# Performance work log

Measured on AMD Instinct MI355X. Metric: run time of the kernel, lower is better.

## Reference

```python
import jax, jax.numpy as jnp
import numpy as np
import math

CHANNELS = 512
OUT_CHANNELS = 512
N_HEADS = 8
WINDOW = 4
K_CH = CHANNELS // N_HEADS


def _conv1x1(x, W, b):
    # x: (B, C_in, T), W: (C_out, C_in), b: (C_out,)
    return jnp.einsum('oc,bct->bot', W, x) + b[None, :, None]


def _get_relative_embeddings(emb, length, window=WINDOW):
    # emb: (H, 2*window+1, k_ch) -> (H, 2*length-1, k_ch)
    pad_length = max(length - (window + 1), 0)
    start = max(window + 1 - length, 0)
    e = jnp.pad(emb, ((0, 0), (pad_length, pad_length), (0, 0))) if pad_length > 0 else emb
    return e[:, start:start + 2 * length - 1]


def _relative_to_absolute(x):
    # x: (B, H, L, 2L-1) -> (B, H, L, L)
    b, h, L, _ = x.shape
    x = jnp.pad(x, ((0, 0), (0, 0), (0, 0), (0, 1)))          # (B,H,L,2L)
    xf = x.reshape(b, h, L * 2 * L)
    xf = jnp.pad(xf, ((0, 0), (0, 0), (L - 1, 0)))
    return xf.reshape(b, h, L + 1, 2 * L - 1)[:, :, :L, L - 1:]


def _absolute_to_relative(x):
    # x: (B, H, L, L) -> (B, H, L, 2L-1)
    b, h, L, _ = x.shape
    x = jnp.pad(x, ((0, 0), (0, 0), (0, 0), (0, L - 1)))       # (B,H,L,2L-1)
    xf = x.reshape(b, h, L * (2 * L - 1))
    xf = jnp.pad(xf, ((0, 0), (0, 0), (L, 0)))
    return xf.reshape(b, h, L, 2 * L)[:, :, :, 1:]


def setup_inputs() -> dict:
    key = jax.random.key(0)
    ks = jax.random.split(key, 16)
    B, C, T = 4, CHANNELS, 1024
    xavier = math.sqrt(2.0 / (C + C))
    rel_std = K_CH ** -0.5
    return {
        'x_q': jax.random.normal(ks[0], (B, C, T), jnp.float32),
        'x_k': jax.random.normal(ks[1], (B, C, T), jnp.float32),
        'x_v': jax.random.normal(ks[2], (B, C, T), jnp.float32),
        'Wq': jax.random.normal(ks[3], (C, C), jnp.float32) * xavier,
        'bq': jnp.zeros((C,), jnp.float32),
        'Wk': jax.random.normal(ks[4], (C, C), jnp.float32) * xavier,
        'bk': jnp.zeros((C,), jnp.float32),
        'Wv': jax.random.normal(ks[5], (C, C), jnp.float32) * xavier,
        'bv': jnp.zeros((C,), jnp.float32),
        'Wo': jax.random.normal(ks[6], (OUT_CHANNELS, C), jnp.float32) * xavier,
        'bo': jnp.zeros((OUT_CHANNELS,), jnp.float32),
        'emb_rel_k': jax.random.normal(ks[7], (N_HEADS, 2 * WINDOW + 1, K_CH), jnp.float32) * rel_std,
        'emb_rel_v': jax.random.normal(ks[8], (N_HEADS, 2 * WINDOW + 1, K_CH), jnp.float32) * rel_std,
    }


def reference(x_q, x_k, x_v, Wq, bq, Wk, bk, Wv, bv, Wo, bo, emb_rel_k, emb_rel_v):
    q = _conv1x1(x_q, Wq, bq)
    k = _conv1x1(x_k, Wk, bk)
    v = _conv1x1(x_v, Wv, bv)
    B, C, T = q.shape
    # (B, C, T) -> (B, H, T, k_ch); head h owns contiguous k_ch channel chunk
    qh = q.reshape(B, N_HEADS, K_CH, T).transpose(0, 1, 3, 2) / math.sqrt(K_CH)
    kh = k.reshape(B, N_HEADS, K_CH, T).transpose(0, 1, 3, 2)
    vh = v.reshape(B, N_HEADS, K_CH, T).transpose(0, 1, 3, 2)
    scores = jnp.einsum('bhtd,bhsd->bhts', qh, kh)              # (B,H,T,T)
    rel_k = _get_relative_embeddings(emb_rel_k, T)              # (H,2T-1,d)
    rel_logits = jnp.einsum('bhtd,hmd->bhtm', qh, rel_k)        # (B,H,T,2T-1)
    scores = scores + _relative_to_absolute(rel_logits)
    attn = jax.nn.softmax(scores, axis=-1)
    ctx = jnp.einsum('bhts,bhsd->bhtd', attn, vh)
    rel_w = _absolute_to_relative(attn)                         # (B,H,T,2T-1)
    rel_v = _get_relative_embeddings(emb_rel_v, T)
    ctx = ctx + jnp.einsum('bhtm,hmd->bhtd', rel_w, rel_v)
    out = ctx.transpose(0, 1, 3, 2).reshape(B, C, T)
    return _conv1x1(out, Wo, bo)
```

## Files before the change

kernel.cpp:

```cpp
#include <hip/hip_runtime.h>

#define T_LEN 1024
#define NH 8
#define DH 64
#define CCH 512
#define LOG2E 1.44269504088896340736f

typedef _Float16 f16;
typedef _Float16 f16x8 __attribute__((ext_vector_type(8)));
typedef _Float16 f16x4 __attribute__((ext_vector_type(4)));
typedef float f32x4 __attribute__((ext_vector_type(4)));

__device__ __forceinline__ void dma16(const void* g, void* l)
{
    __builtin_amdgcn_global_load_lds((const __attribute__((address_space(1))) void*)g,
                                     (__attribute__((address_space(3))) void*)l, 16, 0, 0);
}

__global__ __launch_bounds__(256)
void prep_kernel(const float* __restrict__ x0, const float* __restrict__ x1,
                 const float* __restrict__ x2, const float* __restrict__ W0,
                 const float* __restrict__ W1, const float* __restrict__ W2,
                 const float* __restrict__ W3, f16* __restrict__ o0,
                 f16* __restrict__ o1, f16* __restrict__ o2, f16* __restrict__ w0,
                 f16* __restrict__ w1, f16* __restrict__ w2, f16* __restrict__ w3,
                 int B)
{
    const int z = blockIdx.z;
    if (z < 3 * B) {
        const int t0 = blockIdx.x * 64, c0 = blockIdx.y * 64;
        const int which = z / B, b = z % B;
        const float* x = (which == 0) ? x0 : (which == 1) ? x1 : x2;
        f16* o = (which == 0) ? o0 : (which == 1) ? o1 : o2;

        __shared__ float L[64 * 68];
        const int cl = threadIdx.x & 63, g = threadIdx.x >> 6;
        const float* src = x + ((size_t)(b * CCH + c0 + cl)) * T_LEN + t0 + g * 16;
        #pragma unroll
        for (int j = 0; j < 4; ++j)
            *(float4*)&L[cl * 68 + g * 16 + 4 * j] = *(const float4*)&src[4 * j];
        __syncthreads();
        const int tl = threadIdx.x & 63, cg = (threadIdx.x >> 6) * 16;
        f16 h[16];
        #pragma unroll
        for (int j = 0; j < 16; ++j) h[j] = (f16)L[(cg + j) * 68 + tl];
        f16* dst = o + ((size_t)(b * T_LEN + t0 + tl)) * CCH + c0 + cg;
        *(f16x8*)&dst[0] = *(f16x8*)&h[0];
        *(f16x8*)&dst[8] = *(f16x8*)&h[8];
    } else {
        const int slice = z - 3 * B;
        size_t i = ((size_t)(slice * 128 + blockIdx.y * 16 + blockIdx.x) * 256 + threadIdx.x) * 4;
        const int wi = (int)(i >> 18);
        const size_t off = i & 262143;
        const float* src = (wi == 0) ? W0 : (wi == 1) ? W1 : (wi == 2) ? W2 : W3;
        f16* dst = (wi == 0) ? w0 : (wi == 1) ? w1 : (wi == 2) ? w2 : w3;
        float4 v4 = *(const float4*)&src[off];
        f16x4 h = {(f16)v4.x, (f16)v4.y, (f16)v4.z, (f16)v4.w};
        *(f16x4*)&dst[off] = h;
    }
}

__global__ __launch_bounds__(256)
void proj_qkv(const f16* __restrict__ xq, const f16* __restrict__ xk,
              const f16* __restrict__ xv, const f16* __restrict__ wq,
              const f16* __restrict__ wk, const f16* __restrict__ wv,
              const float* __restrict__ bq, const float* __restrict__ bk,
              const float* __restrict__ bv, f16* __restrict__ qo,
              f16* __restrict__ ko, f16* __restrict__ vo)
{
    const int which = blockIdx.z;
    const f16* X = (which == 0) ? xq : (which == 1) ? xk : xv;
    const f16* W = (which == 0) ? wq : (which == 1) ? wk : wv;
    const float* bias = (which == 0) ? bq : (which == 1) ? bk : bv;
    const float scale = (which == 0) ? 0.125f * LOG2E : 1.0f;

    const int r0 = blockIdx.x * 128;
    const int o0 = blockIdx.y * 64;
    const int tid = threadIdx.x;
    const int w = tid >> 6, lane = tid & 63;
    const int quad = lane >> 4, l15 = lane & 15;

    __shared__ __align__(16) f16 Xs[2][128 * 64];
    __shared__ __align__(16) f16 Ws[2][64 * 64];

    const int srow = tid >> 3;
    const int scol = ((tid & 7) ^ (srow & 7)) << 3;

    const f16* Xg = X + (size_t)(r0 + srow) * CCH + scol;
    const f16* Wg = W + (size_t)(o0 + srow) * CCH + scol;

    #pragma unroll
    for (int j = 0; j < 4; ++j)
        dma16(Xg + (size_t)(32 * j) * CCH, &Xs[0][(size_t)tid * 8 + j * 2048]);
    #pragma unroll
    for (int j = 0; j < 2; ++j)
        dma16(Wg + (size_t)(32 * j) * CCH, &Ws[0][(size_t)tid * 8 + j * 2048]);

    f32x4 acc[8] = {};

    for (int kc = 0; kc < 8; ++kc) {
        __syncthreads();
        if (kc < 7) {
            const int bf = (kc + 1) & 1, c1 = (kc + 1) * 64;
            #pragma unroll
            for (int j = 0; j < 4; ++j)
                dma16(Xg + c1 + (size_t)(32 * j) * CCH, &Xs[bf][(size_t)tid * 8 + j * 2048]);
            #pragma unroll
            for (int j = 0; j < 2; ++j)
                dma16(Wg + c1 + (size_t)(32 * j) * CCH, &Ws[bf][(size_t)tid * 8 + j * 2048]);
        }
        const int cb = kc & 1;
        #pragma unroll
        for (int ks = 0; ks < 2; ++ks) {
            const int sl = ((ks * 4 + quad) ^ (l15 & 7)) << 3;
            f16x8 xf[2], wf[4];
            #pragma unroll
            for (int im = 0; im < 2; ++im)
                xf[im] = *(const f16x8*)&Xs[cb][(32 * w + 16 * im + l15) * 64 + sl];
            #pragma unroll
            for (int cm = 0; cm < 4; ++cm)
                wf[cm] = *(const f16x8*)&Ws[cb][(16 * cm + l15) * 64 + sl];
            if (which < 2) {
                #pragma unroll
                for (int im = 0; im < 2; ++im)
                    #pragma unroll
                    for (int cm = 0; cm < 4; ++cm)
                        acc[im * 4 + cm] = __builtin_amdgcn_mfma_f32_16x16x32_f16(
                            xf[im], wf[cm], acc[im * 4 + cm], 0, 0, 0);
            } else {
                #pragma unroll
                for (int cm = 0; cm < 4; ++cm)
                    #pragma unroll
                    for (int in = 0; in < 2; ++in)
                        acc[cm * 2 + in] = __builtin_amdgcn_mfma_f32_16x16x32_f16(
                            wf[cm], xf[in], acc[cm * 2 + in], 0, 0, 0);
            }
        }
    }

    if (which < 2) {
        f16* out = (which == 0) ? qo : ko;
        float bl[4];
        #pragma unroll
        for (int cm = 0; cm < 4; ++cm) bl[cm] = bias[o0 + 16 * cm + l15];
        #pragma unroll
        for (int im = 0; im < 2; ++im)
            #pragma unroll
            for (int r = 0; r < 4; ++r) {
                size_t row = (size_t)(r0 + 32 * w + 16 * im + 4 * quad + r) * CCH;
                #pragma unroll
                for (int cm = 0; cm < 4; ++cm)
                    out[row + o0 + 16 * cm + l15] =
                        (f16)((acc[im * 4 + cm][r] + bl[cm]) * scale);
            }
    } else {
        const int bb = r0 >> 10, tb = r0 & 1023;
        #pragma unroll
        for (int cm = 0; cm < 4; ++cm) {
            float4 bv4 = *(const float4*)&bias[o0 + 16 * cm + 4 * quad];
            float bl[4] = {bv4.x, bv4.y, bv4.z, bv4.w};
            #pragma unroll
            for (int r = 0; r < 4; ++r) {
                size_t row = ((size_t)(bb * CCH + o0 + 16 * cm + 4 * quad + r)) * T_LEN;
                #pragma unroll
                for (int in = 0; in < 2; ++in)
                    vo[row + tb + 32 * w + 16 * in + l15] =
                        (f16)(acc[cm * 2 + in][r] + bl[r]);
            }
        }
    }
}

__global__ __launch_bounds__(256)
void attn_mfma(const f16* __restrict__ q, const f16* __restrict__ kk,
               const f16* __restrict__ v, const float* __restrict__ ekg,
               const float* __restrict__ evg, f16* __restrict__ ctx)
{
    const int t0 = blockIdx.x * 64, h = blockIdx.y, b = blockIdx.z;
    const int tid = threadIdx.x;
    const int w = tid >> 6, lane = tid & 63;
    const int quad = lane >> 4, l15 = lane & 15;

    __shared__ __align__(16) f16 Qs[4096], Ps[4096];
    __shared__ __align__(16) f16 Ks[2][4096], Vs[2][4096];
    __shared__ float eks[576], evs[576];
    __shared__ float ls[64];

    const int srow = tid >> 3;
    const int scol = ((tid & 7) ^ (srow & 7)) << 3;

    for (int i = tid; i < 576; i += 256) {
        eks[i] = ekg[h * 576 + i];
        evs[i] = evg[h * 576 + i];
    }

    const f16* gk = kk + ((size_t)(b * T_LEN + srow)) * CCH + h * DH + scol;
    const f16* gv = v + ((size_t)(b * CCH + h * DH + srow)) * T_LEN + scol;

    dma16(q + ((size_t)(b * T_LEN + t0 + srow)) * CCH + h * DH + scol, &Qs[(size_t)tid * 8]);
    dma16(q + ((size_t)(b * T_LEN + t0 + srow + 32)) * CCH + h * DH + scol, &Qs[((size_t)tid + 256) * 8]);
    dma16(gk, &Ks[0][(size_t)tid * 8]);
    dma16(gk + (size_t)32 * CCH, &Ks[0][((size_t)tid + 256) * 8]);
    dma16(gv, &Vs[0][(size_t)tid * 8]);
    dma16(gv + (size_t)32 * T_LEN, &Vs[0][((size_t)tid + 256) * 8]);
    __syncthreads();

    f16x8 qf[2];
    #pragma unroll
    for (int ks = 0; ks < 2; ++ks)
        qf[ks] = *(const f16x8*)&Qs[(16 * w + l15) * 64 + (((ks * 4 + quad) ^ (l15 & 7)) << 3)];

    const int myt = 16 * w + l15;
    float Ssum = 0.f;
    f32x4 O[4] = {};

    const bool corner_hi = (blockIdx.x == 0);
    const bool corner_lo = (blockIdx.x == 15);

    for (int it = 0; it < 16; ++it) {
        const int kb = it, cb = it & 1;
        if (it) __syncthreads();

        f32x4 S[4] = {};
        #pragma unroll
        for (int ks = 0; ks < 2; ++ks) {
            #pragma unroll
            for (int ct = 0; ct < 4; ++ct) {
                f16x8 a = *(const f16x8*)&Ks[cb][(16 * ct + l15) * 64 + (((ks * 4 + quad) ^ (l15 & 7)) << 3)];
                S[ct] = __builtin_amdgcn_mfma_f32_16x16x32_f16(a, qf[ks], S[ct], 0, 0, 0);
            }
        }

        if ((corner_hi && kb == 15) || (corner_lo && kb == 0)) {
            const int s0g = kb * 64;
            #pragma unroll
            for (int ct = 0; ct < 4; ++ct)
                #pragma unroll
                for (int r = 0; r < 4; ++r) {
                    int t_g = t0 + myt;
                    int s_g = s0g + 16 * ct + 4 * quad + r;
                    int df = s_g - t_g;
                    if (df >= 1019 && df <= 1023) {
                        const float* ekp = &eks[(df - 1019) * 64];
                        float sacc = 0.f;
                        for (int d = 0; d < 64; ++d)
                            sacc += (float)Qs[myt * 64 + (((d >> 3) ^ (myt & 7)) << 3) + (d & 7)] * ekp[d];
                        S[ct][r] += sacc;
                    } else if (df >= -1023 && df <= -1021) {
                        const float* ekp = &eks[(1029 + df) * 64];
                        const int t2 = myt - 1;
                        float sacc = 0.f;
                        for (int d = 0; d < 64; ++d)
                            sacc += (float)Qs[t2 * 64 + (((d >> 3) ^ (t2 & 7)) << 3) + (d & 7)] * ekp[d];
                        S[ct][r] += sacc;
                    }
                }
        }

        #pragma unroll
        for (int ct = 0; ct < 4; ++ct) {
            f16x4 pk_;
            #pragma unroll
            for (int r = 0; r < 4; ++r) {
                float p = exp2f(S[ct][r]);
                Ssum += p;
                pk_[r] = (f16)p;
            }
            int colh = (((2 * ct + (quad >> 1)) ^ (myt & 7)) << 3) + (quad & 1) * 4;
            *(f16x4*)&Ps[myt * 64 + colh] = pk_;
        }
        __syncthreads();

        if (it < 15) {
            const int nb = cb ^ 1;
            dma16(gk + (size_t)((it + 1) * 64) * CCH, &Ks[nb][(size_t)tid * 8]);
            dma16(gk + (size_t)((it + 1) * 64 + 32) * CCH, &Ks[nb][((size_t)tid + 256) * 8]);
            dma16(gv + (it + 1) * 64, &Vs[nb][(size_t)tid * 8]);
            dma16(gv + (size_t)32 * T_LEN + (it + 1) * 64, &Vs[nb][((size_t)tid + 256) * 8]);
        }

        #pragma unroll
        for (int ks = 0; ks < 2; ++ks) {
            f16x8 a = *(const f16x8*)&Ps[(16 * w + l15) * 64 + (((ks * 4 + quad) ^ (l15 & 7)) << 3)];
            #pragma unroll
            for (int ct = 0; ct < 4; ++ct) {
                f16x8 bf = *(const f16x8*)&Vs[cb][(16 * ct + l15) * 64 + (((ks * 4 + quad) ^ (l15 & 7)) << 3)];
                O[ct] = __builtin_amdgcn_mfma_f32_16x16x32_f16(a, bf, O[ct], 0, 0, 0);
            }
        }

        const int s0g = kb * 64;
        if (s0g <= t0 + 67 && s0g + 63 >= t0 - 4) {
            #pragma unroll
            for (int r = 0; r < 4; ++r) {
                int t_loc = 16 * w + 4 * quad + r;
                int t_g = t0 + t_loc;
                int slo = max(s0g, t_g - 4), shi = min(s0g + 63, t_g + 4);
                for (int s = slo; s <= shi; ++s) {
                    int sl = s - s0g;
                    float p = (float)Ps[t_loc * 64 + (((sl >> 3) ^ (t_loc & 7)) << 3) + (sl & 7)];
                    const float* evp = &evs[(s - t_g + 4) * 64];
                    #pragma unroll
                    for (int ct = 0; ct < 4; ++ct)
                        O[ct][r] += p * evp[16 * ct + l15];
                }
            }
        }
    }

    Ssum += __shfl_xor(Ssum, 16);
    Ssum += __shfl_xor(Ssum, 32);
    if (quad == 0) ls[myt] = 1.0f / Ssum;
    __syncthreads();

    #pragma unroll
    for (int r = 0; r < 4; ++r) {
        const int t_loc = 16 * w + 4 * quad + r;
        const float rl = ls[t_loc];
        size_t rowo = ((size_t)(b * T_LEN + t0 + t_loc)) * CCH + h * DH;
        #pragma unroll
        for (int ct = 0; ct < 4; ++ct)
            ctx[rowo + 16 * ct + l15] = (f16)(O[ct][r] * rl);
    }
}

__global__ __launch_bounds__(256)
void proj_out(const f16* __restrict__ ctx, const f16* __restrict__ Wo,
              const float* __restrict__ bo, float* __restrict__ out)
{
    const int r0 = blockIdx.x * 64;
    const int o0 = blockIdx.y * 64;
    const int tid = threadIdx.x;
    const int w = tid >> 6, lane = tid & 63;
    const int quad = lane >> 4, l15 = lane & 15;

    __shared__ __align__(16) f16 Cs[2][4096];
    __shared__ __align__(16) f16 Ws[2][4096];

    const int srow = tid >> 3;
    const int scol = ((tid & 7) ^ (srow & 7)) << 3;

    const f16* Cg = ctx + (size_t)(r0 + srow) * CCH + scol;
    const f16* Wg = Wo + (size_t)(o0 + srow) * CCH + scol;

    dma16(Cg, &Cs[0][(size_t)tid * 8]);
    dma16(Cg + (size_t)32 * CCH, &Cs[0][((size_t)tid + 256) * 8]);
    dma16(Wg, &Ws[0][(size_t)tid * 8]);
    dma16(Wg + (size_t)32 * CCH, &Ws[0][((size_t)tid + 256) * 8]);

    f32x4 acc[4] = {};

    for (int kc = 0; kc < 8; ++kc) {
        __syncthreads();
        if (kc < 7) {
            const int bf = (kc + 1) & 1, c1 = (kc + 1) * 64;
            dma16(Cg + c1, &Cs[bf][(size_t)tid * 8]);
            dma16(Cg + c1 + (size_t)32 * CCH, &Cs[bf][((size_t)tid + 256) * 8]);
            dma16(Wg + c1, &Ws[bf][(size_t)tid * 8]);
            dma16(Wg + c1 + (size_t)32 * CCH, &Ws[bf][((size_t)tid + 256) * 8]);
        }
        const int cb = kc & 1;
        #pragma unroll
        for (int ks = 0; ks < 2; ++ks) {
            const int sl = ((ks * 4 + quad) ^ (l15 & 7)) << 3;
            f16x8 cf = *(const f16x8*)&Cs[cb][(16 * w + l15) * 64 + sl];
            #pragma unroll
            for (int cm = 0; cm < 4; ++cm) {
                f16x8 wf = *(const f16x8*)&Ws[cb][(16 * cm + l15) * 64 + sl];
                acc[cm] = __builtin_amdgcn_mfma_f32_16x16x32_f16(wf, cf, acc[cm], 0, 0, 0);
            }
        }
    }

    const int bb = r0 >> 10, tb = r0 & 1023;
    #pragma unroll
    for (int cm = 0; cm < 4; ++cm) {
        float4 bv4 = *(const float4*)&bo[o0 + 16 * cm + 4 * quad];
        float bl[4] = {bv4.x, bv4.y, bv4.z, bv4.w};
        #pragma unroll
        for (int r = 0; r < 4; ++r) {
            size_t row = ((size_t)(bb * CCH + o0 + 16 * cm + 4 * quad + r)) * T_LEN;
            out[row + tb + 16 * w + l15] = acc[cm][r] + bl[r];
        }
    }
}

extern "C" void kernel_launch(void* const* d_in, const int* in_sizes, int n_in,
                              void* d_out, int out_size, void* d_ws, size_t ws_size,
                              hipStream_t stream)
{
    const float* x_q = (const float*)d_in[0];
    const float* x_k = (const float*)d_in[1];
    const float* x_v = (const float*)d_in[2];
    const float* Wq  = (const float*)d_in[3];
    const float* bq  = (const float*)d_in[4];
    const float* Wk  = (const float*)d_in[5];
    const float* bk  = (const float*)d_in[6];
    const float* Wv  = (const float*)d_in[7];
    const float* bv  = (const float*)d_in[8];
    const float* Wo  = (const float*)d_in[9];
    const float* bo  = (const float*)d_in[10];
    const float* erk = (const float*)d_in[11];
    const float* erv = (const float*)d_in[12];

    const int B = in_sizes[0] / (CCH * T_LEN);
    const size_t te = (size_t)B * CCH * T_LEN;
    const size_t we = (size_t)CCH * CCH;

    f16* p = (f16*)d_ws;
    f16* xTq = p; p += te;
    f16* xTk = p; p += te;
    f16* xTv = p; p += te;
    f16* wqh = p; p += we;
    f16* wkh = p; p += we;
    f16* wvh = p; p += we;
    f16* woh = p; p += we;
    f16* qh  = p; p += te;
    f16* kh  = p; p += te;
    f16* vh  = p; p += te;
    f16* ch  = p; p += te;

    dim3 blk(256);
    prep_kernel<<<dim3(16, 8, 3 * B + 8), blk, 0, stream>>>(
        x_q, x_k, x_v, Wq, Wk, Wv, Wo, xTq, xTk, xTv, wqh, wkh, wvh, woh, B);
    proj_qkv<<<dim3(B * 8, 8, 3), blk, 0, stream>>>(
        xTq, xTk, xTv, wqh, wkh, wvh, bq, bk, bv, qh, kh, vh);
    attn_mfma<<<dim3(T_LEN / 64, NH, B), blk, 0, stream>>>(
        qh, kh, vh, erk, erv, ch);
    proj_out<<<dim3(B * 16, 8), blk, 0, stream>>>(
        ch, woh, bo, (float*)d_out);
}
```

Baseline: 152.7 us.

## Load activation fragments directly into registers and hoist K/V prefetch in attention

In the QKV and output projection kernels, the activation operand is no longer staged through LDS. Each wave loads its own MFMA fragments straight from global memory into registers, prefetching the next k-chunk one iteration ahead, while weights stay double-buffered in LDS. This cuts LDS footprint and traffic, at the cost of more register pressure and uncoalesced-ish 16-byte global loads. In attention, the next K/V tile DMA is issued at the top of the iteration and one barrier between the P write and the PV product is removed. Dropping that barrier risks reading Ps rows before they are written, though each wave appears to read only its own rows.

```diff
diff --git a/kernel.cpp b/kernel.cpp
--- a/kernel.cpp
+++ b/kernel.cpp
@@ -80,21 +80,22 @@
     const int w = tid >> 6, lane = tid & 63;
     const int quad = lane >> 4, l15 = lane & 15;
 
-    __shared__ __align__(16) f16 Xs[2][128 * 64];
-    __shared__ __align__(16) f16 Ws[2][64 * 64];
+    __shared__ __align__(16) f16 Ws[2][4096];
 
     const int srow = tid >> 3;
     const int scol = ((tid & 7) ^ (srow & 7)) << 3;
-
-    const f16* Xg = X + (size_t)(r0 + srow) * CCH + scol;
     const f16* Wg = W + (size_t)(o0 + srow) * CCH + scol;
 
+    dma16(Wg, &Ws[0][(size_t)tid * 8]);
+    dma16(Wg + (size_t)32 * CCH, &Ws[0][((size_t)tid + 256) * 8]);
+
+    const f16* xp = X + (size_t)(r0 + 32 * w + l15) * CCH + quad * 8;
+    f16x8 xf[2][2];
     #pragma unroll
-    for (int j = 0; j < 4; ++j)
-        dma16(Xg + (size_t)(32 * j) * CCH, &Xs[0][(size_t)tid * 8 + j * 2048]);
-    #pragma unroll
-    for (int j = 0; j < 2; ++j)
-        dma16(Wg + (size_t)(32 * j) * CCH, &Ws[0][(size_t)tid * 8 + j * 2048]);
+    for (int ks = 0; ks < 2; ++ks)
+        #pragma unroll
+        for (int im = 0; im < 2; ++im)
+            xf[ks][im] = *(const f16x8*)&xp[(size_t)(16 * im) * CCH + ks * 32];
 
     f32x4 acc[8] = {};
 
@@ -102,21 +103,22 @@
         __syncthreads();
         if (kc < 7) {
             const int bf = (kc + 1) & 1, c1 = (kc + 1) * 64;
-            #pragma unroll
-            for (int j = 0; j < 4; ++j)
-                dma16(Xg + c1 + (size_t)(32 * j) * CCH, &Xs[bf][(size_t)tid * 8 + j * 2048]);
-            #pragma unroll
-            for (int j = 0; j < 2; ++j)
-                dma16(Wg + c1 + (size_t)(32 * j) * CCH, &Ws[bf][(size_t)tid * 8 + j * 2048]);
-        }
+            dma16(Wg + c1, &Ws[bf][(size_t)tid * 8]);
+            dma16(Wg + c1 + (size_t)32 * CCH, &Ws[bf][((size_t)tid + 256) * 8]);
+        }
+        const int nk = ((kc + 1) & 7) * 64;
+        f16x8 xn[2][2];
+        #pragma unroll
+        for (int ks = 0; ks < 2; ++ks)
+            #pragma unroll
+            for (int im = 0; im < 2; ++im)
+                xn[ks][im] = *(const f16x8*)&xp[(size_t)(16 * im) * CCH + nk + ks * 32];
+
         const int cb = kc & 1;
         #pragma unroll
         for (int ks = 0; ks < 2; ++ks) {
             const int sl = ((ks * 4 + quad) ^ (l15 & 7)) << 3;
-            f16x8 xf[2], wf[4];
-            #pragma unroll
-            for (int im = 0; im < 2; ++im)
-                xf[im] = *(const f16x8*)&Xs[cb][(32 * w + 16 * im + l15) * 64 + sl];
+            f16x8 wf[4];
             #pragma unroll
             for (int cm = 0; cm < 4; ++cm)
                 wf[cm] = *(const f16x8*)&Ws[cb][(16 * cm + l15) * 64 + sl];
@@ -126,16 +128,21 @@
                     #pragma unroll
                     for (int cm = 0; cm < 4; ++cm)
                         acc[im * 4 + cm] = __builtin_amdgcn_mfma_f32_16x16x32_f16(
-                            xf[im], wf[cm], acc[im * 4 + cm], 0, 0, 0);
+                            xf[ks][im], wf[cm], acc[im * 4 + cm], 0, 0, 0);
             } else {
                 #pragma unroll
                 for (int cm = 0; cm < 4; ++cm)
                     #pragma unroll
                     for (int in = 0; in < 2; ++in)
                         acc[cm * 2 + in] = __builtin_amdgcn_mfma_f32_16x16x32_f16(
-                            wf[cm], xf[in], acc[cm * 2 + in], 0, 0, 0);
-            }
-        }
+                            wf[cm], xf[ks][in], acc[cm * 2 + in], 0, 0, 0);
+            }
+        }
+        #pragma unroll
+        for (int ks = 0; ks < 2; ++ks)
+            #pragma unroll
+            for (int im = 0; im < 2; ++im)
+                xf[ks][im] = xn[ks][im];
     }
 
     if (which < 2) {
@@ -220,6 +227,14 @@
     for (int it = 0; it < 16; ++it) {
         const int kb = it, cb = it & 1;
         if (it) __syncthreads();
+
+        if (it < 15) {
+            const int nb = cb ^ 1;
+            dma16(gk + (size_t)((it + 1) * 64) * CCH, &Ks[nb][(size_t)tid * 8]);
+            dma16(gk + (size_t)((it + 1) * 64 + 32) * CCH, &Ks[nb][((size_t)tid + 256) * 8]);
+            dma16(gv + (it + 1) * 64, &Vs[nb][(size_t)tid * 8]);
+            dma16(gv + (size_t)32 * T_LEN + (it + 1) * 64, &Vs[nb][((size_t)tid + 256) * 8]);
+        }
 
         f32x4 S[4] = {};
         #pragma unroll
@@ -269,15 +284,6 @@
             int colh = (((2 * ct + (quad >> 1)) ^ (myt & 7)) << 3) + (quad & 1) * 4;
             *(f16x4*)&Ps[myt * 64 + colh] = pk_;
         }
-        __syncthreads();
-
-        if (it < 15) {
-            const int nb = cb ^ 1;
-            dma16(gk + (size_t)((it + 1) * 64) * CCH, &Ks[nb][(size_t)tid * 8]);
-            dma16(gk + (size_t)((it + 1) * 64 + 32) * CCH, &Ks[nb][((size_t)tid + 256) * 8]);
-            dma16(gv + (it + 1) * 64, &Vs[nb][(size_t)tid * 8]);
-            dma16(gv + (size_t)32 * T_LEN + (it + 1) * 64, &Vs[nb][((size_t)tid + 256) * 8]);
-        }
 
         #pragma unroll
         for (int ks = 0; ks < 2; ++ks) {
@@ -334,19 +340,20 @@
     const int w = tid >> 6, lane = tid & 63;
     const int quad = lane >> 4, l15 = lane & 15;
 
-    __shared__ __align__(16) f16 Cs[2][4096];
     __shared__ __align__(16) f16 Ws[2][4096];
 
     const int srow = tid >> 3;
     const int scol = ((tid & 7) ^ (srow & 7)) << 3;
-
-    const f16* Cg = ctx + (size_t)(r0 + srow) * CCH + scol;
     const f16* Wg = Wo + (size_t)(o0 + srow) * CCH + scol;
 
-    dma16(Cg, &Cs[0][(size_t)tid * 8]);
-    dma16(Cg + (size_t)32 * CCH, &Cs[0][((size_t)tid + 256) * 8]);
     dma16(Wg, &Ws[0][(size_t)tid * 8]);
     dma16(Wg + (size_t)32 * CCH, &Ws[0][((size_t)tid + 256) * 8]);
+
+    const f16* cp = ctx + (size_t)(r0 + 16 * w + l15) * CCH + quad * 8;
+    f16x8 cf[2];
+    #pragma unroll
+    for (int ks = 0; ks < 2; ++ks)
+        cf[ks] = *(const f16x8*)&cp[ks * 32];
 
     f32x4 acc[4] = {};
 
@@ -354,22 +361,27 @@
         __syncthreads();
         if (kc < 7) {
             const int bf = (kc + 1) & 1, c1 = (kc + 1) * 64;
-            dma16(Cg + c1, &Cs[bf][(size_t)tid * 8]);
-            dma16(Cg + c1 + (size_t)32 * CCH, &Cs[bf][((size_t)tid + 256) * 8]);
             dma16(Wg + c1, &Ws[bf][(size_t)tid * 8]);
             dma16(Wg + c1 + (size_t)32 * CCH, &Ws[bf][((size_t)tid + 256) * 8]);
         }
+        const int nk = ((kc + 1) & 7) * 64;
+        f16x8 cn[2];
+        #pragma unroll
+        for (int ks = 0; ks < 2; ++ks)
+            cn[ks] = *(const f16x8*)&cp[nk + ks * 32];
+
         const int cb = kc & 1;
         #pragma unroll
         for (int ks = 0; ks < 2; ++ks) {
             const int sl = ((ks * 4 + quad) ^ (l15 & 7)) << 3;
-            f16x8 cf = *(const f16x8*)&Cs[cb][(16 * w + l15) * 64 + sl];
             #pragma unroll
             for (int cm = 0; cm < 4; ++cm) {
                 f16x8 wf = *(const f16x8*)&Ws[cb][(16 * cm + l15) * 64 + sl];
-                acc[cm] = __builtin_amdgcn_mfma_f32_16x16x32_f16(wf, cf, acc[cm], 0, 0, 0);
-            }
-        }
+                acc[cm] = __builtin_amdgcn_mfma_f32_16x16x32_f16(wf, cf[ks], acc[cm], 0, 0, 0);
+            }
+        }
+        cf[0] = cn[0];
+        cf[1] = cn[1];
     }
 
     const int bb = r0 >> 10, tb = r0 & 1023;
```

New measurement: 152.7 us. About the same (-0.0%).

## Enlarge projection GEMM tiles to 128x128 and prefetch K/V earlier in attention

Applied to the files above, without the earlier changes.

The QKV and output projection kernels now use 128x128 output tiles, with each wave computing a 64x64 sub-tile (4x4 MFMAs). This raises operand reuse per LDS load but drops LDS double buffering in favour of load-then-sync per K chunk. The grids shrink accordingly, to 384 blocks for QKV and 128 for the output projection. In attention, the next K/V tile DMA is issued at the start of each iteration and the intermediate barrier before the PV product is removed, giving more overlap but risking a race on the Ps buffer writes versus reads.

```diff
diff --git a/kernel.cpp b/kernel.cpp
--- a/kernel.cpp
+++ b/kernel.cpp
@@ -75,13 +75,15 @@
     const float scale = (which == 0) ? 0.125f * LOG2E : 1.0f;
 
     const int r0 = blockIdx.x * 128;
-    const int o0 = blockIdx.y * 64;
+    const int o0 = blockIdx.y * 128;
     const int tid = threadIdx.x;
     const int w = tid >> 6, lane = tid & 63;
     const int quad = lane >> 4, l15 = lane & 15;
-
-    __shared__ __align__(16) f16 Xs[2][128 * 64];
-    __shared__ __align__(16) f16 Ws[2][64 * 64];
+    const int a  = w >> 1;
+    const int b2 = w & 1;
+
+    __shared__ __align__(16) f16 Xs[128 * 64];
+    __shared__ __align__(16) f16 Wsh[128 * 64];
 
     const int srow = tid >> 3;
     const int scol = ((tid & 7) ^ (srow & 7)) << 3;
@@ -89,51 +91,45 @@
     const f16* Xg = X + (size_t)(r0 + srow) * CCH + scol;
     const f16* Wg = W + (size_t)(o0 + srow) * CCH + scol;
 
-    #pragma unroll
-    for (int j = 0; j < 4; ++j)
-        dma16(Xg + (size_t)(32 * j) * CCH, &Xs[0][(size_t)tid * 8 + j * 2048]);
-    #pragma unroll
-    for (int j = 0; j < 2; ++j)
-        dma16(Wg + (size_t)(32 * j) * CCH, &Ws[0][(size_t)tid * 8 + j * 2048]);
-
-    f32x4 acc[8] = {};
+    const int ax = (which < 2) ? a : b2;
+    const int aw = (which < 2) ? b2 : a;
+
+    f32x4 acc[4][4] = {};
 
     for (int kc = 0; kc < 8; ++kc) {
+        if (kc) __syncthreads();
+        const int c1 = kc * 64;
+        #pragma unroll
+        for (int jj = 0; jj < 4; ++jj) {
+            dma16(Xg + c1 + (size_t)(32 * jj) * CCH, &Xs[((size_t)tid + 256 * jj) * 8]);
+            dma16(Wg + c1 + (size_t)(32 * jj) * CCH, &Wsh[((size_t)tid + 256 * jj) * 8]);
+        }
         __syncthreads();
-        if (kc < 7) {
-            const int bf = (kc + 1) & 1, c1 = (kc + 1) * 64;
-            #pragma unroll
-            for (int j = 0; j < 4; ++j)
-                dma16(Xg + c1 + (size_t)(32 * j) * CCH, &Xs[bf][(size_t)tid * 8 + j * 2048]);
-            #pragma unroll
-            for (int j = 0; j < 2; ++j)
-                dma16(Wg + c1 + (size_t)(32 * j) * CCH, &Ws[bf][(size_t)tid * 8 + j * 2048]);
-        }
-        const int cb = kc & 1;
+
         #pragma unroll
         for (int ks = 0; ks < 2; ++ks) {
             const int sl = ((ks * 4 + quad) ^ (l15 & 7)) << 3;
-            f16x8 xf[2], wf[4];
-            #pragma unroll
-            for (int im = 0; im < 2; ++im)
-                xf[im] = *(const f16x8*)&Xs[cb][(32 * w + 16 * im + l15) * 64 + sl];
-            #pragma unroll
-            for (int cm = 0; cm < 4; ++cm)
-                wf[cm] = *(const f16x8*)&Ws[cb][(16 * cm + l15) * 64 + sl];
+            f16x8 xf[4], wf[4];
+            #pragma unroll
+            for (int i = 0; i < 4; ++i)
+                xf[i] = *(const f16x8*)&Xs[(64 * ax + 16 * i + l15) * 64 + sl];
+            #pragma unroll
+            for (int j = 0; j < 4; ++j)
+                wf[j] = *(const f16x8*)&Wsh[(64 * aw + 16 * j + l15) * 64 + sl];
             if (which < 2) {
                 #pragma unroll
-                for (int im = 0; im < 2; ++im)
+                for (int i = 0; i < 4; ++i)
                     #pragma unroll
-                    for (int cm = 0; cm < 4; ++cm)
-                        acc[im * 4 + cm] = __builtin_amdgcn_mfma_f32_16x16x32_f16(
-                            xf[im], wf[cm], acc[im * 4 + cm], 0, 0, 0);
+                    for (int j = 0; j < 4; ++j)
+                        acc[i][j] = __builtin_amdgcn_mfma_f32_16x16x32_f16(
+                            xf[i], wf[j], acc[i][j], 0, 0, 0);
             } else {
                 #pragma unroll
-                for (int cm = 0; cm < 4; ++cm)
+                for (int i = 0; i < 4; ++i)
                     #pragma unroll
-                    for (int in = 0; in < 2; ++in)
-                        acc[cm * 2 + in] = __builtin_amdgcn_mfma_f32_16x16x32_f16(
-                            wf[cm], xf[in], acc[cm * 2 + in], 0, 0, 0);
+                    for (int j = 0; j < 4; ++j)
+                        acc[i][j] = __builtin_amdgcn_mfma_f32_16x16x32_f16(
+                            wf[i], xf[j], acc[i][j], 0, 0, 0);
             }
         }
     }
@@ -142,30 +138,30 @@
         f16* out = (which == 0) ? qo : ko;
         float bl[4];
         #pragma unroll
-        for (int cm = 0; cm < 4; ++cm) bl[cm] = bias[o0 + 16 * cm + l15];
-        #pragma unroll
-        for (int im = 0; im < 2; ++im)
+        for (int j = 0; j < 4; ++j) bl[j] = bias[o0 + 64 * b2 + 16 * j + l15];
+        #pragma unroll
+        for (int i = 0; i < 4; ++i)
             #pragma unroll
             for (int r = 0; r < 4; ++r) {
-                size_t row = (size_t)(r0 + 32 * w + 16 * im + 4 * quad + r) * CCH;
-                #pragma unroll
-                for (int cm = 0; cm < 4; ++cm)
-                    out[row + o0 + 16 * cm + l15] =
-                        (f16)((acc[im * 4 + cm][r] + bl[cm]) * scale);
+                size_t row = (size_t)(r0 + 64 * a + 16 * i + 4 * quad + r) * CCH;
+                #pragma unroll
+                for (int j = 0; j < 4; ++j)
+                    out[row + o0 + 64 * b2 + 16 * j + l15] =
+                        (f16)((acc[i][j][r] + bl[j]) * scale);
             }
     } else {
         const int bb = r0 >> 10, tb = r0 & 1023;
         #pragma unroll
-        for (int cm = 0; cm < 4; ++cm) {
-            float4 bv4 = *(const float4*)&bias[o0 + 16 * cm + 4 * quad];
+        for (int i = 0; i < 4; ++i) {
+            float4 bv4 = *(const float4*)&bias[o0 + 64 * a + 16 * i + 4 * quad];
             float bl[4] = {bv4.x, bv4.y, bv4.z, bv4.w};
             #pragma unroll
             for (int r = 0; r < 4; ++r) {
-                size_t row = ((size_t)(bb * CCH + o0 + 16 * cm + 4 * quad + r)) * T_LEN;
-                #pragma unroll
-                for (int in = 0; in < 2; ++in)
-                    vo[row + tb + 32 * w + 16 * in + l15] =
-                        (f16)(acc[cm * 2 + in][r] + bl[r]);
+                size_t row = ((size_t)(bb * CCH + o0 + 64 * a + 16 * i + 4 * quad + r)) * T_LEN;
+                #pragma unroll
+                for (int j = 0; j < 4; ++j)
+                    vo[row + tb + 64 * b2 + 16 * j + l15] =
+                        (f16)(acc[i][j][r] + bl[r]);
             }
         }
     }
@@ -221,13 +217,21 @@
         const int kb = it, cb = it & 1;
         if (it) __syncthreads();
 
+        if (it < 15) {
+            const int nb = cb ^ 1;
+            dma16(gk + (size_t)((it + 1) * 64) * CCH, &Ks[nb][(size_t)tid * 8]);
+            dma16(gk + (size_t)((it + 1) * 64 + 32) * CCH, &Ks[nb][((size_t)tid + 256) * 8]);
+            dma16(gv + (it + 1) * 64, &Vs[nb][(size_t)tid * 8]);
+            dma16(gv + (size_t)32 * T_LEN + (it + 1) * 64, &Vs[nb][((size_t)tid + 256) * 8]);
+        }
+
         f32x4 S[4] = {};
         #pragma unroll
         for (int ks = 0; ks < 2; ++ks) {
             #pragma unroll
             for (int ct = 0; ct < 4; ++ct) {
-                f16x8 a = *(const f16x8*)&Ks[cb][(16 * ct + l15) * 64 + (((ks * 4 + quad) ^ (l15 & 7)) << 3)];
-                S[ct] = __builtin_amdgcn_mfma_f32_16x16x32_f16(a, qf[ks], S[ct], 0, 0, 0);
+                f16x8 aa = *(const f16x8*)&Ks[cb][(16 * ct + l15) * 64 + (((ks * 4 + quad) ^ (l15 & 7)) << 3)];
+                S[ct] = __builtin_amdgcn_mfma_f32_16x16x32_f16(aa, qf[ks], S[ct], 0, 0, 0);
             }
         }
 
@@ -269,23 +273,14 @@
             int colh = (((2 * ct + (quad >> 1)) ^ (myt & 7)) << 3) + (quad & 1) * 4;
             *(f16x4*)&Ps[myt * 64 + colh] = pk_;
         }
-        __syncthreads();
-
-        if (it < 15) {
-            const int nb = cb ^ 1;
-            dma16(gk + (size_t)((it + 1) * 64) * CCH, &Ks[nb][(size_t)tid * 8]);
-            dma16(gk + (size_t)((it + 1) * 64 + 32) * CCH, &Ks[nb][((size_t)tid + 256) * 8]);
-            dma16(gv + (it + 1) * 64, &Vs[nb][(size_t)tid * 8]);
-            dma16(gv + (size_t)32 * T_LEN + (it + 1) * 64, &Vs[nb][((size_t)tid + 256) * 8]);
-        }
 
         #pragma unroll
         for (int ks = 0; ks < 2; ++ks) {
-            f16x8 a = *(const f16x8*)&Ps[(16 * w + l15) * 64 + (((ks * 4 + quad) ^ (l15 & 7)) << 3)];
+            f16x8 aa = *(const f16x8*)&Ps[(16 * w + l15) * 64 + (((ks * 4 + quad) ^ (l15 & 7)) << 3)];
             #pragma unroll
             for (int ct = 0; ct < 4; ++ct) {
                 f16x8 bf = *(const f16x8*)&Vs[cb][(16 * ct + l15) * 64 + (((ks * 4 + quad) ^ (l15 & 7)) << 3)];
-                O[ct] = __builtin_amdgcn_mfma_f32_16x16x32_f16(a, bf, O[ct], 0, 0, 0);
+                O[ct] = __builtin_amdgcn_mfma_f32_16x16x32_f16(aa, bf, O[ct], 0, 0, 0);
             }
         }
 
@@ -328,14 +323,16 @@
 void proj_out(const f16* __restrict__ ctx, const f16* __restrict__ Wo,
               const float* __restrict__ bo, float* __restrict__ out)
 {
-    const int r0 = blockIdx.x * 64;
-    const int o0 = blockIdx.y * 64;
+    const int r0 = blockIdx.x * 128;
+    const int o0 = blockIdx.y * 128;
     const int tid = threadIdx.x;
     const int w = tid >> 6, lane = tid & 63;
     const int quad = lane >> 4, l15 = lane & 15;
-
-    __shared__ __align__(16) f16 Cs[2][4096];
-    __shared__ __align__(16) f16 Ws[2][4096];
+    const int a  = w >> 1;
+    const int b2 = w & 1;
+
+    __shared__ __align__(16) f16 Cs[128 * 64];
+    __shared__ __align__(16) f16 Wsh[128 * 64];
 
     const int srow = tid >> 3;
     const int scol = ((tid & 7) ^ (srow & 7)) << 3;
@@ -343,44 +340,48 @@
     const f16* Cg = ctx + (size_t)(r0 + srow) * CCH + scol;
     const f16* Wg = Wo + (size_t)(o0 + srow) * CCH + scol;
 
-    dma16(Cg, &Cs[0][(size_t)tid * 8]);
-    dma16(Cg + (size_t)32 * CCH, &Cs[0][((size_t)tid + 256) * 8]);
-    dma16(Wg, &Ws[0][(size_t)tid * 8]);
-    dma16(Wg + (size_t)32 * CCH, &Ws[0][((size_t)tid + 256) * 8]);
-
-    f32x4 acc[4] = {};
+    f32x4 acc[4][4] = {};
 
     for (int kc = 0; kc < 8; ++kc) {
+        if (kc) __syncthreads();
+        const int c1 = kc * 64;
+        #pragma unroll
+        for (int jj = 0; jj < 4; ++jj) {
+            dma16(Cg + c1 + (size_t)(32 * jj) * CCH, &Cs[((size_t)tid + 256 * jj) * 8]);
+            dma16(Wg + c1 + (size_t)(32 * jj) * CCH, &Wsh[((size_t)tid + 256 * jj) * 8]);
+        }
         __syncthreads();
-        if (kc < 7) {
-            const int bf = (kc + 1) & 1, c1 = (kc + 1) * 64;
-            dma16(Cg + c1, &Cs[bf][(size_t)tid * 8]);
-            dma16(Cg + c1 + (size_t)32 * CCH, &Cs[bf][((size_t)tid + 256) * 8]);
-            dma16(Wg + c1, &Ws[bf][(size_t)tid * 8]);
-            dma16(Wg + c1 + (size_t)32 * CCH, &Ws[bf][((size_t)tid + 256) * 8]);
-        }
-        const int cb = kc & 1;
+
         #pragma unroll
         for (int ks = 0; ks < 2; ++ks) {
             const int sl = ((ks * 4 + quad) ^ (l15 & 7)) << 3;
-            f16x8 cf = *(const f16x8*)&Cs[cb][(16 * w + l15) * 64 + sl];
-            #pragma unroll
-            for (int cm = 0; cm < 4; ++cm) {
-                f16x8 wf = *(const f16x8*)&Ws[cb][(16 * cm + l15) * 64 + sl];
-                acc[cm] = __builtin_amdgcn_mfma_f32_16x16x32_f16(wf, cf, acc[cm], 0, 0, 0);
-            }
+            f16x8 wf[4], cf[4];
+            #pragma unroll
+            for (int i = 0; i < 4; ++i)
+                wf[i] = *(const f16x8*)&Wsh[(64 * a + 16 * i + l15) * 64 + sl];
+            #pragma unroll
+            for (int j = 0; j < 4; ++j)
+                cf[j] = *(const f16x8*)&Cs[(64 * b2 + 16 * j + l15) * 64 + sl];
+            #pragma unroll
+            for (int i = 0; i < 4; ++i)
+                #pragma unroll
+                for (int j = 0; j < 4; ++j)
+                    acc[i][j] = __builtin_amdgcn_mfma_f32_16x16x32_f16(
+                        wf[i], cf[j], acc[i][j], 0, 0, 0);
         }
     }
 
     const int bb = r0 >> 10, tb = r0 & 1023;
     #pragma unroll
-    for (int cm = 0; cm < 4; ++cm) {
-        float4 bv4 = *(const float4*)&bo[o0 + 16 * cm + 4 * quad];
+    for (int i = 0; i < 4; ++i) {
+        float4 bv4 = *(const float4*)&bo[o0 + 64 * a + 16 * i + 4 * quad];
         float bl[4] = {bv4.x, bv4.y, bv4.z, bv4.w};
         #pragma unroll
         for (int r = 0; r < 4; ++r) {
-            size_t row = ((size_t)(bb * CCH + o0 + 16 * cm + 4 * quad + r)) * T_LEN;
-            out[row + tb + 16 * w + l15] = acc[cm][r] + bl[r];
+            size_t row = ((size_t)(bb * CCH + o0 + 64 * a + 16 * i + 4 * quad + r)) * T_LEN;
+            #pragma unroll
+            for (int j = 0; j < 4; ++j)
+                out[row + tb + 64 * b2 + 16 * j + l15] = acc[i][j][r] + bl[r];
         }
     }
 }
@@ -423,10 +424,10 @@
     dim3 blk(256);
     prep_kernel<<<dim3(16, 8, 3 * B + 8), blk, 0, stream>>>(
         x_q, x_k, x_v, Wq, Wk, Wv, Wo, xTq, xTk, xTv, wqh, wkh, wvh, woh, B);
-    proj_qkv<<<dim3(B * 8, 8, 3), blk, 0, stream>>>(
+    proj_qkv<<<dim3(B * 8, 4, 3), blk, 0, stream>>>(
         xTq, xTk, xTv, wqh, wkh, wvh, bq, bk, bv, qh, kh, vh);
     attn_mfma<<<dim3(T_LEN / 64, NH, B), blk, 0, stream>>>(
         qh, kh, vh, erk, erv, ch);
-    proj_out<<<dim3(B * 16, 8), blk, 0, stream>>>(
+    proj_out<<<dim3(B * 8, 4), blk, 0, stream>>>(
         ch, woh, bo, (float*)d_out);
 }
```

Result: no change. 152.1 us (-0.4%).
